# Kernel tuning notes

Hardware: AMD Instinct MI355X
Metric: run time of the kernel (lower is better)

## Reference

```python
import jax, jax.numpy as jnp
import numpy as np
from jax import lax

RANK = 8
ALPHA = 16.0
SCALING = ALPHA / RANK  # 2.0
C_IN, C_OUT, KH, KW = 128, 256, 3, 3


def setup_inputs() -> dict:
    key = jax.random.key(0)
    k1, k2, k3, k4, k5 = jax.random.split(key, 5)
    x = jax.random.normal(k1, (16, C_IN, 64, 64), dtype=jnp.float32)
    W = jax.random.normal(k2, (C_OUT, C_IN, KH, KW), dtype=jnp.float32) * 0.05
    b = jax.random.normal(k3, (C_OUT,), dtype=jnp.float32) * 0.05
    lora_A = jax.random.normal(k4, (RANK, C_IN * KH * KW), dtype=jnp.float32) * 0.02
    lora_B = jax.random.normal(k5, (C_OUT, RANK), dtype=jnp.float32) * 0.02
    return {"x": x, "W": W, "b": b, "lora_A": lora_A, "lora_B": lora_B}


def _conv(x, w, stride=(1, 1), padding=((1, 1), (1, 1))):
    return lax.conv_general_dilated(
        x, w, window_strides=stride, padding=padding,
        dimension_numbers=("NCHW", "OIHW", "NCHW"))


def reference(x, W, b, lora_A, lora_B):
    # Base (frozen) conv: [B, C_out, H, W]
    base_out = _conv(x, W) + b[None, :, None, None]
    # LoRA path. The torch code does im2col -> (BL, C_in*kh*kw) @ A.T @ B.T.
    # Because unfold flattens patches channel-major as (C_in, kh, kw), the
    # identical math is: rank-r conv with A reshaped as [rank, C_in, kh, kw],
    # then a 1x1 mix with B. Same result, no im2col materialization.
    A_k = lora_A.reshape(RANK, C_IN, KH, KW)
    h = _conv(x, A_k)                                   # [B, rank, H, W]
    lora_out = jnp.einsum("brhw,or->bohw", h, lora_B) * SCALING
    return base_out + lora_out
```

## Files before the change

kernel.cpp:

```cpp
#include <hip/hip_runtime.h>
#include <hip/hip_bf16.h>


#define CIN   128
#define COUT  256
#define NBAT  16
#define HPAD  66
#define WPAD  66

typedef __bf16 bf16x8 __attribute__((ext_vector_type(8)));
typedef float f32x4 __attribute__((ext_vector_type(4)));

#define XPAD_ELEMS ((size_t)NBAT * HPAD * WPAD * CIN)
#define XPAD_BYTES (XPAD_ELEMS * 2)
#define WT_ELEMS   ((size_t)9 * COUT * CIN)
#define WS_NEED    (XPAD_BYTES + WT_ELEMS * 2)

typedef __attribute__((address_space(1))) void gvoid;
typedef __attribute__((address_space(3))) void lvoid;

__device__ __forceinline__ void load_lds16(const void* g, void* l) {
    __builtin_amdgcn_global_load_lds((gvoid*)g, (lvoid*)l, 16, 0, 0);
}

__global__ void pad_prep(const float* __restrict__ x, __bf16* __restrict__ xpad,
                         const float* __restrict__ W, const float* __restrict__ lA,
                         const float* __restrict__ lB, __hip_bfloat16* __restrict__ Wt) {
    __shared__ float tile[128][66];
    const int t = threadIdx.x;

    if (blockIdx.x >= 1024) {
        const int idx = (blockIdx.x - 1024) * 256 + t;
        const int c = idx & 127;
        const int o = idx >> 7;
        float lb[8];
#pragma unroll
        for (int r = 0; r < 8; ++r) lb[r] = lB[o * 8 + r];
#pragma unroll
        for (int tap = 0; tap < 9; ++tap) {
            float acc = W[(o * 128 + c) * 9 + tap];
            float s = 0.f;
#pragma unroll
            for (int r = 0; r < 8; ++r)
                s += lb[r] * lA[r * 1152 + c * 9 + tap];
            Wt[tap * 32768 + idx] = __float2bfloat16(acc + 2.0f * s);
        }
        return;
    }

    const int n = blockIdx.x >> 6;
    const int h = blockIdx.x & 63;
    const float* src = x + (size_t)n * 128 * 4096 + (size_t)h * 64;
#pragma unroll
    for (int i = 0; i < 8; ++i) {
        int g  = i * 256 + t;
        int c  = g >> 4;
        int w4 = (g & 15) * 4;
        const float4 v = *reinterpret_cast<const float4*>(src + (size_t)c * 4096 + w4);
        const int wb = w4 ^ (((c >> 3) & 7) << 2);
        tile[c][wb + 0] = v.x; tile[c][wb + 1] = v.y;
        tile[c][wb + 2] = v.z; tile[c][wb + 3] = v.w;
    }
    __syncthreads();
    __bf16* dst = xpad + ((size_t)(n * 66 + h + 1) * 66 + 1) * 128;
#pragma unroll
    for (int i = 0; i < 4; ++i) {
        int g  = i * 256 + t;
        int w  = g >> 4;
        int c0 = (g & 15) * 8;
        const int swr = ((c0 >> 3) & 7) << 2;
        bf16x8 v;
#pragma unroll
        for (int j = 0; j < 8; ++j) v[j] = (__bf16)tile[c0 + j][w ^ swr];
        *reinterpret_cast<bf16x8*>(dst + (size_t)w * 128 + c0) = v;
    }
    bf16x8 z = {};
    __bf16* rowbase = xpad + (size_t)(n * 66 + h + 1) * 66 * 128;
    if (t < 32) {
        int ww = (t < 16) ? 0 : 65;
        int c0 = (t & 15) * 8;
        *reinterpret_cast<bf16x8*>(rowbase + (size_t)ww * 128 + c0) = z;
    }
    if (h == 0 || h == 63) {
        __bf16* hrow = xpad + (size_t)(n * 66 + (h == 0 ? 0 : 65)) * 66 * 128;
        for (int i = t; i < 66 * 16; i += 256)
            *reinterpret_cast<bf16x8*>(hrow + (size_t)i * 8) = z;
    }
}

__global__ void __launch_bounds__(512, 2) conv_mfma(
    const __bf16* __restrict__ xpad, const __bf16* __restrict__ Wt,
    const float* __restrict__ bias, float* __restrict__ out) {
    __shared__ __align__(16) __bf16 lds[65536];

    const int tid  = threadIdx.x;
    const int wv   = tid >> 6;
    const int lane = tid & 63;

    const int n  = blockIdx.x >> 4;
    const int h0 = (blockIdx.x & 15) << 2;

    const int swz = ((lane >> 3) << 7) + ((((lane & 7) ^ (lane >> 3)) & 7) << 3);

    const __bf16* aG[4];
    const __bf16* bG[4];
#pragma unroll
    for (int j = 0; j < 4; ++j) {
        const int r0 = wv * 32 + j * 8;
        aG[j] = Wt + (size_t)r0 * 128 + swz;
        bG[j] = xpad + (((size_t)(n * 66 + h0 + (r0 >> 6)) * 66 + (r0 & 63)) * 128) + swz;
    }

    const int wo   = (wv >> 2) << 7;
    const int wpix = (wv & 3) << 6;
    const int a_rd = (wo + (lane & 15)) << 6;
    const int b_rd = (wpix + (lane & 15)) << 6;
    int qo[2];
#pragma unroll
    for (int s = 0; s < 2; ++s)
        qo[s] = ((((lane >> 4) + s * 4) ^ (lane & 7)) & 7) << 3;

    f32x4 acc[8][4] = {};

#pragma unroll
    for (int j = 0; j < 4; ++j) {
        load_lds16(aG[j], lds + (wv * 32 + j * 8) * 64);
        load_lds16(bG[j], lds + 32768 + (wv * 32 + j * 8) * 64);
    }

#pragma unroll
    for (int t = 0; t < 18; ++t) {
        asm volatile("s_waitcnt vmcnt(0) lgkmcnt(0)" ::: "memory");
        __builtin_amdgcn_sched_barrier(0);
        __builtin_amdgcn_s_barrier();

        if (t + 1 < 18) {
            const int t1   = t + 1;
            const int tap1 = t1 >> 1, cb1 = t1 & 1;
            const int ao = tap1 * 32768 + cb1 * 64;
            const int bo = ((tap1 / 3) * 66 + (tap1 % 3)) * 128 + cb1 * 64;
            __bf16* Ad = lds + (t1 & 1) * 16384;
            __bf16* Bd = lds + 32768 + (t1 & 1) * 16384;
#pragma unroll
            for (int j = 0; j < 4; ++j) {
                load_lds16(aG[j] + ao, Ad + (wv * 32 + j * 8) * 64);
                load_lds16(bG[j] + bo, Bd + (wv * 32 + j * 8) * 64);
            }
        }

        const __bf16* Ab = lds + (t & 1) * 16384 + a_rd;
        const __bf16* Bb = lds + 32768 + (t & 1) * 16384 + b_rd;
#pragma unroll
        for (int s = 0; s < 2; ++s) {
            bf16x8 af[8], bfr[4];
#pragma unroll
            for (int ni = 0; ni < 4; ++ni)
                bfr[ni] = *reinterpret_cast<const bf16x8*>(Bb + (ni << 10) + qo[s]);
#pragma unroll
            for (int mi = 0; mi < 8; ++mi)
                af[mi] = *reinterpret_cast<const bf16x8*>(Ab + (mi << 10) + qo[s]);
            __builtin_amdgcn_s_setprio(1);
#pragma unroll
            for (int mi = 0; mi < 8; ++mi)
#pragma unroll
                for (int ni = 0; ni < 4; ++ni)
                    acc[mi][ni] = __builtin_amdgcn_mfma_f32_16x16x32_bf16(
                        af[mi], bfr[ni], acc[mi][ni], 0, 0, 0);
            __builtin_amdgcn_s_setprio(0);
        }
    }

    const int col  = lane & 15;
    const int orow = (lane >> 4) << 2;
    const int h    = h0 + (wpix >> 6);
#pragma unroll
    for (int mi = 0; mi < 8; ++mi) {
        const int obm = wo + mi * 16 + orow;
#pragma unroll
        for (int j = 0; j < 4; ++j) {
            const int o = obm + j;
            const float bj = bias[o];
            float* orow_ptr = out + (((size_t)n * 256 + o) * 64 + h) * 64;
#pragma unroll
            for (int ni = 0; ni < 4; ++ni)
                orow_ptr[ni * 16 + col] = acc[mi][ni][j] + bj;
        }
    }
}

__global__ void conv_naive(const float* __restrict__ x, const float* __restrict__ W,
                           const float* __restrict__ b, const float* __restrict__ lA,
                           const float* __restrict__ lB, float* __restrict__ out) {
    int idx = blockIdx.x * 256 + threadIdx.x;
    int w = idx & 63, h = (idx >> 6) & 63, o = (idx >> 12) & 255, n = idx >> 20;
    float acc = b[o];
    float hr[8] = {0, 0, 0, 0, 0, 0, 0, 0};
    for (int c = 0; c < 128; ++c)
        for (int kh = 0; kh < 3; ++kh) {
            int hy = h + kh - 1;
            if (hy < 0 || hy > 63) continue;
            for (int kw = 0; kw < 3; ++kw) {
                int wx = w + kw - 1;
                if (wx < 0 || wx > 63) continue;
                float xv = x[((n * 128 + c) * 64 + hy) * 64 + wx];
                int ka = c * 9 + kh * 3 + kw;
                acc += W[(o * 128 + c) * 9 + kh * 3 + kw] * xv;
#pragma unroll
                for (int r = 0; r < 8; ++r) hr[r] += lA[r * 1152 + ka] * xv;
            }
        }
    float ls = 0.f;
#pragma unroll
    for (int r = 0; r < 8; ++r) ls += lB[o * 8 + r] * hr[r];
    out[idx] = acc + 2.0f * ls;
}

extern "C" void kernel_launch(void* const* d_in, const int* in_sizes, int n_in,
                              void* d_out, int out_size, void* d_ws, size_t ws_size,
                              hipStream_t stream) {
    const float* x  = (const float*)d_in[0];
    const float* W  = (const float*)d_in[1];
    const float* b  = (const float*)d_in[2];
    const float* lA = (const float*)d_in[3];
    const float* lB = (const float*)d_in[4];
    float* out = (float*)d_out;

    if (ws_size < WS_NEED) {
        conv_naive<<<out_size / 256, 256, 0, stream>>>(x, W, b, lA, lB, out);
        return;
    }

    __bf16* xpad = (__bf16*)d_ws;
    __hip_bfloat16* Wt = (__hip_bfloat16*)((char*)d_ws + XPAD_BYTES);

    pad_prep<<<1024 + 128, 256, 0, stream>>>(x, xpad, W, lA, lB, Wt);
    conv_mfma<<<256, 512, 0, stream>>>(xpad, (const __bf16*)Wt, b, out);
}
```

Baseline: 129.1 us.

## Deepen conv MFMA pipeline to four LDS stages with 32-channel K chunks

Restructures the implicit-GEMM main loop from a double-buffered 64-channel K step (18 iterations) into a 4-buffer ring of 32-channel K chunks (36 iterations) with three stages prefetched ahead. The wait on global-to-LDS loads becomes a partial vmcnt so several loads stay in flight across the barrier, meant to hide global memory latency better. The LDS layout and swizzle change to match 32-element rows. In exchange there are twice as many barriers and smaller MFMA batches per barrier. The change also relies on correct vmcnt accounting across the stages.

```diff
diff --git a/kernel.cpp b/kernel.cpp
--- a/kernel.cpp
+++ b/kernel.cpp
@@ -100,75 +100,85 @@
     const int n  = blockIdx.x >> 4;
     const int h0 = (blockIdx.x & 15) << 2;
 
-    const int swz = ((lane >> 3) << 7) + ((((lane & 7) ^ (lane >> 3)) & 7) << 3);
-
-    const __bf16* aG[4];
-    const __bf16* bG[4];
-#pragma unroll
-    for (int j = 0; j < 4; ++j) {
-        const int r0 = wv * 32 + j * 8;
-        aG[j] = Wt + (size_t)r0 * 128 + swz;
-        bG[j] = xpad + (((size_t)(n * 66 + h0 + (r0 >> 6)) * 66 + (r0 & 63)) * 128) + swz;
+    const int lrow = lane >> 2;
+    const int lswz = (((lane & 3) ^ (lrow & 3)) << 3);
+    const __bf16* aG[2];
+    const __bf16* bG[2];
+#pragma unroll
+    for (int j = 0; j < 2; ++j) {
+        const int r0 = j * 128 + wv * 16;
+        aG[j] = Wt + (r0 + lrow) * 128 + lswz;
+        bG[j] = xpad + (((size_t)(n * 66 + h0 + (r0 >> 6)) * 66 + (r0 & 63) + lrow) * 128) + lswz;
     }
 
     const int wo   = (wv >> 2) << 7;
     const int wpix = (wv & 3) << 6;
-    const int a_rd = (wo + (lane & 15)) << 6;
-    const int b_rd = (wpix + (lane & 15)) << 6;
-    int qo[2];
-#pragma unroll
-    for (int s = 0; s < 2; ++s)
-        qo[s] = ((((lane >> 4) + s * 4) ^ (lane & 7)) & 7) << 3;
+    const int fr   = lane & 15;
+    const int fphys = (((lane >> 4) ^ (lane & 3)) << 3);
+    const int a_rd = (wo + fr) * 32 + fphys;
+    const int b_rd = (wpix + fr) * 32 + fphys;
 
     f32x4 acc[8][4] = {};
 
-#pragma unroll
-    for (int j = 0; j < 4; ++j) {
-        load_lds16(aG[j], lds + (wv * 32 + j * 8) * 64);
-        load_lds16(bG[j], lds + 32768 + (wv * 32 + j * 8) * 64);
-    }
-
-#pragma unroll
-    for (int t = 0; t < 18; ++t) {
-        asm volatile("s_waitcnt vmcnt(0) lgkmcnt(0)" ::: "memory");
+#define STAGE(u) do {                                                          \
+        const int tap_ = (u) >> 2, cb_ = (u) & 3;                              \
+        const int kh_ = (tap_ >= 6) ? 2 : (tap_ >= 3 ? 1 : 0);                 \
+        const int kw_ = tap_ - kh_ * 3;                                        \
+        const int ao_ = tap_ * 32768 + cb_ * 32;                               \
+        const int bo_ = (kh_ * 66 + kw_) * 128 + cb_ * 32;                     \
+        const int lb_ = ((u) & 3) * 8192;                                      \
+        load_lds16(aG[0] + ao_, lds + lb_ + (wv * 16) * 32);                   \
+        load_lds16(aG[1] + ao_, lds + lb_ + (128 + wv * 16) * 32);             \
+        load_lds16(bG[0] + bo_, lds + 32768 + lb_ + (wv * 16) * 32);           \
+        load_lds16(bG[1] + bo_, lds + 32768 + lb_ + (128 + wv * 16) * 32);     \
+    } while (0)
+
+#define COMPUTE(t) do {                                                        \
+        const int lb_ = ((t) & 3) * 8192;                                      \
+        const __bf16* Ab = lds + lb_ + a_rd;                                   \
+        const __bf16* Bb = lds + 32768 + lb_ + b_rd;                           \
+        bf16x8 af[8], bfr[4];                                                  \
+        _Pragma("unroll")                                                      \
+        for (int ni = 0; ni < 4; ++ni)                                         \
+            bfr[ni] = *reinterpret_cast<const bf16x8*>(Bb + ni * 512);         \
+        _Pragma("unroll")                                                      \
+        for (int mi = 0; mi < 8; ++mi)                                         \
+            af[mi] = *reinterpret_cast<const bf16x8*>(Ab + mi * 512);          \
+        __builtin_amdgcn_s_setprio(1);                                         \
+        _Pragma("unroll")                                                      \
+        for (int mi = 0; mi < 8; ++mi)                                         \
+            _Pragma("unroll")                                                  \
+            for (int ni = 0; ni < 4; ++ni)                                     \
+                acc[mi][ni] = __builtin_amdgcn_mfma_f32_16x16x32_bf16(         \
+                    af[mi], bfr[ni], acc[mi][ni], 0, 0, 0);                    \
+        __builtin_amdgcn_s_setprio(0);                                         \
+    } while (0)
+
+    STAGE(0); STAGE(1); STAGE(2);
+
+    for (int t = 0; t < 33; ++t) {
+        asm volatile("s_waitcnt vmcnt(8)" ::: "memory");
         __builtin_amdgcn_sched_barrier(0);
         __builtin_amdgcn_s_barrier();
-
-        if (t + 1 < 18) {
-            const int t1   = t + 1;
-            const int tap1 = t1 >> 1, cb1 = t1 & 1;
-            const int ao = tap1 * 32768 + cb1 * 64;
-            const int bo = ((tap1 / 3) * 66 + (tap1 % 3)) * 128 + cb1 * 64;
-            __bf16* Ad = lds + (t1 & 1) * 16384;
-            __bf16* Bd = lds + 32768 + (t1 & 1) * 16384;
-#pragma unroll
-            for (int j = 0; j < 4; ++j) {
-                load_lds16(aG[j] + ao, Ad + (wv * 32 + j * 8) * 64);
-                load_lds16(bG[j] + bo, Bd + (wv * 32 + j * 8) * 64);
-            }
-        }
-
-        const __bf16* Ab = lds + (t & 1) * 16384 + a_rd;
-        const __bf16* Bb = lds + 32768 + (t & 1) * 16384 + b_rd;
-#pragma unroll
-        for (int s = 0; s < 2; ++s) {
-            bf16x8 af[8], bfr[4];
-#pragma unroll
-            for (int ni = 0; ni < 4; ++ni)
-                bfr[ni] = *reinterpret_cast<const bf16x8*>(Bb + (ni << 10) + qo[s]);
-#pragma unroll
-            for (int mi = 0; mi < 8; ++mi)
-                af[mi] = *reinterpret_cast<const bf16x8*>(Ab + (mi << 10) + qo[s]);
-            __builtin_amdgcn_s_setprio(1);
-#pragma unroll
-            for (int mi = 0; mi < 8; ++mi)
-#pragma unroll
-                for (int ni = 0; ni < 4; ++ni)
-                    acc[mi][ni] = __builtin_amdgcn_mfma_f32_16x16x32_bf16(
-                        af[mi], bfr[ni], acc[mi][ni], 0, 0, 0);
-            __builtin_amdgcn_s_setprio(0);
-        }
-    }
+        __builtin_amdgcn_sched_barrier(0);
+        STAGE(t + 3);
+        COMPUTE(t);
+    }
+    asm volatile("s_waitcnt vmcnt(8)" ::: "memory");
+    __builtin_amdgcn_sched_barrier(0);
+    __builtin_amdgcn_s_barrier();
+    COMPUTE(33);
+    asm volatile("s_waitcnt vmcnt(4)" ::: "memory");
+    __builtin_amdgcn_sched_barrier(0);
+    __builtin_amdgcn_s_barrier();
+    COMPUTE(34);
+    asm volatile("s_waitcnt vmcnt(0)" ::: "memory");
+    __builtin_amdgcn_sched_barrier(0);
+    __builtin_amdgcn_s_barrier();
+    COMPUTE(35);
+
+#undef STAGE
+#undef COMPUTE
 
     const int col  = lane & 15;
     const int orow = (lane >> 4) << 2;
```

New measurement: 134.5 us. 4.2% more time.
